# Performance work log

Measured on AMD Instinct MI355X. Metric: run time of the kernel, lower is better.

## Reference

```python
import jax, jax.numpy as jnp
import numpy as np

# Module constants (match init_kwargs)
H = 16            # num_heads
K = 64            # max_kernel_size
MAX_FREQ = 16.0
MIN_FREQ = 1.0
HALF_S = 16       # int(32**(1/1)) // 2
S = 2 * HALF_S + 1  # 33 sample offsets: -16..16
MAX_RECEPTIVE = HALF_S * MAX_FREQ  # 256.0


def setup_inputs() -> dict:
    key = jax.random.key(0)
    ks = jax.random.split(key, 6)
    B, L, C = 1, 4096, 1024
    x = jax.random.normal(ks[0], (B, L, C), dtype=jnp.float32)
    # Learned params (random small scale so offsets/kernels vary; torch inits
    # wave_proj to zeros but that degenerates the math under test).
    Ww = jax.random.normal(ks[1], (2 * H, C), dtype=jnp.float32) * 0.02
    bw = jnp.zeros((2 * H,), dtype=jnp.float32)
    Wk = jax.random.normal(ks[2], (H * K, C), dtype=jnp.float32) * 0.02
    bk = jnp.zeros((H * K,), dtype=jnp.float32)
    Wo = jax.random.normal(ks[3], (C, C), dtype=jnp.float32) * 0.02
    return {"x": x, "Ww": Ww, "bw": bw, "Wk": Wk, "bk": bk, "Wo": Wo}


def reference(x, Ww, bw, Wk, bk, Wo):
    B, L, C = x.shape
    D = C // H
    dt = x.dtype
    grid = jnp.arange(-HALF_S, HALF_S + 1, dtype=dt)  # (S,)

    # Predict per-position frequency / phase (averaged over heads)
    wp = jax.nn.silu(x @ Ww.T + bw).reshape(B, L, 2, H)
    freq = jax.nn.sigmoid(wp[:, :, 0]) * (MAX_FREQ - MIN_FREQ) + MIN_FREQ  # (B,L,H)
    phase = jnp.tanh(wp[:, :, 1]) * MAX_FREQ
    freq_avg = freq.mean(-1)    # (B,L)
    phase_avg = phase.mean(-1)  # (B,L)

    # Sample positions & gather indices
    rel_pos = grid[None, None, :] * freq_avg[..., None] + phase_avg[..., None]  # (B,L,S)
    centers = jnp.arange(L, dtype=dt)
    sample_pos = centers[None, :, None] + rel_pos                               # (B,L,S)
    valid = (sample_pos >= 0) & (sample_pos < L)
    sample_idx = jnp.clip(sample_pos.astype(jnp.int32), 0, L - 1)               # trunc toward 0, like torch .long()

    # Gather values: (B,L,S,C) -> (B,L,H,S,D)
    values = jax.vmap(lambda xf, idx: xf[idx])(x, sample_idx)
    values = values.reshape(B, L, S, H, D).transpose(0, 1, 3, 2, 4)

    # Kernel profile, linearly interpolated to sample positions
    kernel_max = jax.nn.silu(x @ Wk.T + bk).reshape(B, L, H, K)
    norm_pos = jnp.clip((rel_pos + MAX_RECEPTIVE) / (2.0 * MAX_RECEPTIVE), 0.0, 1.0)
    idx_float = norm_pos * (K - 1)                       # (B,L,S)
    idx_floor = jnp.clip(idx_float.astype(jnp.int32), 0, K - 2)
    w_ceil = (idx_float - idx_floor.astype(dt))[:, :, None, :]  # (B,L,1,S)
    w_floor = 1.0 - w_ceil
    ifl = jnp.broadcast_to(idx_floor[:, :, None, :], (B, L, H, S))
    k_floor = jnp.take_along_axis(kernel_max, ifl, axis=-1)
    k_ceil = jnp.take_along_axis(kernel_max, ifl + 1, axis=-1)
    kernel = (k_floor * w_floor + k_ceil * w_ceil) * valid[:, :, None, :].astype(dt)
    kernel = kernel / (kernel.sum(-1, keepdims=True) + 1e-8)

    out = jnp.einsum('blhsd,blhs->blhd', values, kernel).reshape(B, L, C)
    out = jax.nn.silu(out @ Wo.T)
    return out
```

## Files before the change

kernel.cpp:

```cpp
#include <hip/hip_runtime.h>
#include <math.h>

#define LDIM 4096
#define CDIM 1024
#define HDIM 16
#define KDIM 64
#define SDIM 33
#define HALF_SS 16
#define MAXF 16.0f
#define MINF 1.0f
#define MAXR 256.0f

__device__ __forceinline__ float sigmoid_np(float z) {
  float e = (float)exp(-(double)z);
  return __fdiv_rn(1.0f, __fadd_rn(1.0f, e));
}
__device__ __forceinline__ float silu_f(float z) {
  return __fmul_rn(z, sigmoid_np(z));
}

__device__ __forceinline__ float np_pairwise_sum(const float* a, int n) {
  float r[8];
#pragma unroll
  for (int j = 0; j < 8; ++j) r[j] = a[j];
  int i = 8;
  for (; i + 8 <= n; i += 8)
#pragma unroll
    for (int j = 0; j < 8; ++j) r[j] = __fadd_rn(r[j], a[i + j]);
  float res = __fadd_rn(__fadd_rn(__fadd_rn(r[0], r[1]), __fadd_rn(r[2], r[3])),
                        __fadd_rn(__fadd_rn(r[4], r[5]), __fadd_rn(r[6], r[7])));
  for (; i < n; ++i) res = __fadd_rn(res, a[i]);
  return res;
}

__global__ __launch_bounds__(256) void wave_kernel(
    const float* __restrict__ x, const float* __restrict__ Ww,
    const float* __restrict__ bw, float* __restrict__ fa, float* __restrict__ pa) {
  __shared__ float xs[CDIM];
  __shared__ float wp[2 * HDIM];
  int l = blockIdx.x;
  int tid = threadIdx.x;
  const float* xrow = x + (size_t)l * CDIM;
  for (int c = tid; c < CDIM; c += 256) xs[c] = xrow[c];
  __syncthreads();
  int j = tid >> 3, sub = tid & 7;
  const float* wrow = Ww + j * CDIM;
  double acc = 0.0;
  for (int c = sub; c < CDIM; c += 8) acc += (double)xs[c] * (double)wrow[c];
  for (int off = 4; off; off >>= 1) acc += __shfl_down(acc, off, 8);
  if (sub == 0) {
    float v32 = (float)(acc + (double)bw[j]);
    wp[j] = silu_f(v32);
  }
  __syncthreads();
  if (tid == 0) {
    float fv[HDIM], pv[HDIM];
    for (int h = 0; h < HDIM; ++h) {
      fv[h] = __fadd_rn(__fmul_rn(sigmoid_np(wp[h]), MAXF - MINF), MINF);
      float t32 = (float)tanh((double)wp[HDIM + h]);
      pv[h] = __fmul_rn(t32, MAXF);
    }
    fa[l] = __fdiv_rn(np_pairwise_sum(fv, HDIM), (float)HDIM);
    pa[l] = __fdiv_rn(np_pairwise_sum(pv, HDIM), (float)HDIM);
  }
}

__global__ __launch_bounds__(256) void gemm_bt_silu_f64(
    const float* __restrict__ A, const float* __restrict__ B,
    const float* __restrict__ bias, float* __restrict__ Cout,
    int M, int N, int Kd) {
  __shared__ double Asd[16][128];
  __shared__ double Bsd[16][64];
  int tid = threadIdx.x;
  int tx = tid & 15, ty = tid >> 4;
  int m0 = blockIdx.y * 128, n0 = blockIdx.x * 64;
  double acc[8][4] = {};
  for (int kt = 0; kt < Kd; kt += 16) {
#pragma unroll
    for (int q = 0; q < 2; ++q) {
      int e = tid + 256 * q;
      int row = e >> 2, kq = (e & 3) * 4;
      float4 va = *(const float4*)(A + (size_t)(m0 + row) * Kd + kt + kq);
      Asd[kq + 0][row] = (double)va.x; Asd[kq + 1][row] = (double)va.y;
      Asd[kq + 2][row] = (double)va.z; Asd[kq + 3][row] = (double)va.w;
    }
    {
      int row = tid >> 2, kq = (tid & 3) * 4;
      float4 vb = *(const float4*)(B + (size_t)(n0 + row) * Kd + kt + kq);
      Bsd[kq + 0][row] = (double)vb.x; Bsd[kq + 1][row] = (double)vb.y;
      Bsd[kq + 2][row] = (double)vb.z; Bsd[kq + 3][row] = (double)vb.w;
    }
    __syncthreads();
#pragma unroll
    for (int kk = 0; kk < 16; ++kk) {
      double a[8], b[4];
#pragma unroll
      for (int i = 0; i < 8; ++i) a[i] = Asd[kk][ty * 8 + i];
#pragma unroll
      for (int j2 = 0; j2 < 4; ++j2) b[j2] = Bsd[kk][tx * 4 + j2];
#pragma unroll
      for (int i = 0; i < 8; ++i)
#pragma unroll
        for (int j2 = 0; j2 < 4; ++j2) acc[i][j2] += a[i] * b[j2];
    }
    __syncthreads();
  }
#pragma unroll
  for (int i = 0; i < 8; ++i) {
    int mm = m0 + ty * 8 + i;
#pragma unroll
    for (int j2 = 0; j2 < 4; ++j2) {
      int nn = n0 + tx * 4 + j2;
      float v32 = (float)acc[i][j2];
      v32 = __fadd_rn(v32, bias[nn]);
      Cout[(size_t)mm * N + nn] = silu_f(v32);
    }
  }
}

__global__ __launch_bounds__(256) void gemm_bt_silu_f32(
    const float* __restrict__ A, const float* __restrict__ B,
    float* __restrict__ Cout, int M, int N, int Kd) {
  __shared__ float Asf[16][128];
  __shared__ float Bsf[16][128];
  int tid = threadIdx.x;
  int tx = tid & 15, ty = tid >> 4;
  int m0 = blockIdx.y * 128, n0 = blockIdx.x * 128;
  float acc[8][8] = {};
  for (int kt = 0; kt < Kd; kt += 16) {
#pragma unroll
    for (int q = 0; q < 2; ++q) {
      int e = tid + 256 * q;
      int row = e >> 2, kq = (e & 3) * 4;
      float4 va = *(const float4*)(A + (size_t)(m0 + row) * Kd + kt + kq);
      Asf[kq + 0][row] = va.x; Asf[kq + 1][row] = va.y;
      Asf[kq + 2][row] = va.z; Asf[kq + 3][row] = va.w;
      float4 vb = *(const float4*)(B + (size_t)(n0 + row) * Kd + kt + kq);
      Bsf[kq + 0][row] = vb.x; Bsf[kq + 1][row] = vb.y;
      Bsf[kq + 2][row] = vb.z; Bsf[kq + 3][row] = vb.w;
    }
    __syncthreads();
#pragma unroll
    for (int kk = 0; kk < 16; ++kk) {
      float4 a0 = *(const float4*)&Asf[kk][ty * 8];
      float4 a1 = *(const float4*)&Asf[kk][ty * 8 + 4];
      float4 b0 = *(const float4*)&Bsf[kk][tx * 8];
      float4 b1 = *(const float4*)&Bsf[kk][tx * 8 + 4];
      float a[8] = {a0.x, a0.y, a0.z, a0.w, a1.x, a1.y, a1.z, a1.w};
      float b[8] = {b0.x, b0.y, b0.z, b0.w, b1.x, b1.y, b1.z, b1.w};
#pragma unroll
      for (int i = 0; i < 8; ++i)
#pragma unroll
        for (int j2 = 0; j2 < 8; ++j2) acc[i][j2] += a[i] * b[j2];
    }
    __syncthreads();
  }
#pragma unroll
  for (int i = 0; i < 8; ++i) {
    int mm = m0 + ty * 8 + i;
#pragma unroll
    for (int j2 = 0; j2 < 8; ++j2) {
      int nn = n0 + tx * 8 + j2;
      Cout[(size_t)mm * N + nn] = silu_f(acc[i][j2]);
    }
  }
}

__global__ __launch_bounds__(256) void conv_kernel(
    const float* __restrict__ x, const float* __restrict__ km,
    const float* __restrict__ fa, const float* __restrict__ pa,
    float* __restrict__ conv) {
  int l = blockIdx.x;
  int tid = threadIdx.x;
  __shared__ int s_idx[SDIM];
  __shared__ int s_ifl[SDIM];
  __shared__ float s_wc[SDIM];
  __shared__ float s_val[SDIM];
  __shared__ float kern[HDIM][SDIM];
  __shared__ float s_den[HDIM];
  if (tid < SDIM) {
    float f = fa[l], p = pa[l];
    float rel = __fadd_rn(__fmul_rn((float)(tid - HALF_SS), f), p);
    float pos = __fadd_rn((float)l, rel);
    bool valid = (pos >= 0.f) && (pos < (float)LDIM);
    int idx = (int)pos;
    idx = min(max(idx, 0), LDIM - 1);
    s_idx[tid] = idx;
    s_val[tid] = valid ? 1.f : 0.f;
    float np_ = __fdiv_rn(__fadd_rn(rel, MAXR), 2.f * MAXR);
    np_ = fminf(fmaxf(np_, 0.f), 1.f);
    float idxf = __fmul_rn(np_, (float)(KDIM - 1));
    int ifl = (int)idxf;
    ifl = min(max(ifl, 0), KDIM - 2);
    s_ifl[tid] = ifl;
    s_wc[tid] = __fsub_rn(idxf, (float)ifl);
  }
  __syncthreads();
  for (int t = tid; t < HDIM * SDIM; t += 256) {
    int h = t / SDIM, s = t - h * SDIM;
    const float* kb = km + (size_t)l * CDIM + h * KDIM;
    float wc = s_wc[s];
    float wf = __fsub_rn(1.f, wc);
    float v = __fadd_rn(__fmul_rn(kb[s_ifl[s]], wf), __fmul_rn(kb[s_ifl[s] + 1], wc));
    kern[h][s] = __fmul_rn(v, s_val[s]);
  }
  __syncthreads();
  if (tid < HDIM) {
    float sum = np_pairwise_sum(&kern[tid][0], SDIM);
    s_den[tid] = __fadd_rn(sum, 1e-8f);
  }
  __syncthreads();
  for (int t = tid; t < HDIM * SDIM; t += 256) {
    int h = t / SDIM, s = t - h * SDIM;
    kern[h][s] = __fdiv_rn(kern[h][s], s_den[h]);
  }
  __syncthreads();
  float acc[4] = {0.f, 0.f, 0.f, 0.f};
  for (int s = 0; s < SDIM; ++s) {
    const float* xr = x + (size_t)s_idx[s] * CDIM;
#pragma unroll
    for (int q = 0; q < 4; ++q) {
      int c = tid + q * 256;
      acc[q] = __fadd_rn(acc[q], __fmul_rn(xr[c], kern[c >> 6][s]));
    }
  }
#pragma unroll
  for (int q = 0; q < 4; ++q) {
    int c = tid + q * 256;
    conv[(size_t)l * CDIM + c] = acc[q];
  }
}

extern "C" void kernel_launch(void* const* d_in, const int* in_sizes, int n_in,
                              void* d_out, int out_size, void* d_ws, size_t ws_size,
                              hipStream_t stream) {
  const float* x  = (const float*)d_in[0];
  const float* Ww = (const float*)d_in[1];
  const float* bw = (const float*)d_in[2];
  const float* Wk = (const float*)d_in[3];
  const float* bk = (const float*)d_in[4];
  const float* Wo = (const float*)d_in[5];
  float* out = (float*)d_out;

  float* fa   = (float*)d_ws;
  float* pa   = fa + LDIM;
  float* km   = pa + LDIM;
  float* conv = km + (size_t)LDIM * CDIM;

  wave_kernel<<<LDIM, 256, 0, stream>>>(x, Ww, bw, fa, pa);

  dim3 kmgrid(CDIM / 64, LDIM / 128);
  gemm_bt_silu_f64<<<kmgrid, 256, 0, stream>>>(x, Wk, bk, km, LDIM, CDIM, CDIM);

  conv_kernel<<<LDIM, 256, 0, stream>>>(x, km, fa, pa, conv);

  dim3 ogrid(CDIM / 128, LDIM / 128);
  gemm_bt_silu_f32<<<ogrid, 256, 0, stream>>>(conv, Wo, out, LDIM, CDIM, CDIM);
}
```

Baseline: 521.3 us.

## Double-buffer shared tiles and shrink GEMM tiles to 64x64 in both GEMMs

Both the f64 kernel-profile GEMM and the f32 output GEMM now use double-buffered shared-memory tiles: the next K-slice is prefetched into registers while the current one is computed, which leaves one barrier per iteration. Block tiles shrink to 64x64 with padded shared arrays and vectorized shared reads and global stores. The aim is to hide global-load latency, cut bank conflicts and put more blocks on the device. In exchange each thread does fewer FMAs per shared load, so arithmetic intensity is lower, which may hurt the f32 GEMM.

```diff
diff --git a/kernel.cpp b/kernel.cpp
--- a/kernel.cpp
+++ b/kernel.cpp
@@ -69,100 +69,143 @@
     const float* __restrict__ A, const float* __restrict__ B,
     const float* __restrict__ bias, float* __restrict__ Cout,
     int M, int N, int Kd) {
-  __shared__ double Asd[16][128];
-  __shared__ double Bsd[16][64];
+  __shared__ double Asd[2][16][66];
+  __shared__ double Bsd[2][16][66];
   int tid = threadIdx.x;
-  int tx = tid & 15, ty = tid >> 4;
-  int m0 = blockIdx.y * 128, n0 = blockIdx.x * 64;
-  double acc[8][4] = {};
-  for (int kt = 0; kt < Kd; kt += 16) {
-#pragma unroll
-    for (int q = 0; q < 2; ++q) {
-      int e = tid + 256 * q;
-      int row = e >> 2, kq = (e & 3) * 4;
-      float4 va = *(const float4*)(A + (size_t)(m0 + row) * Kd + kt + kq);
-      Asd[kq + 0][row] = (double)va.x; Asd[kq + 1][row] = (double)va.y;
-      Asd[kq + 2][row] = (double)va.z; Asd[kq + 3][row] = (double)va.w;
-    }
-    {
-      int row = tid >> 2, kq = (tid & 3) * 4;
-      float4 vb = *(const float4*)(B + (size_t)(n0 + row) * Kd + kt + kq);
-      Bsd[kq + 0][row] = (double)vb.x; Bsd[kq + 1][row] = (double)vb.y;
-      Bsd[kq + 2][row] = (double)vb.z; Bsd[kq + 3][row] = (double)vb.w;
+  int tx = tid & 31;
+  int ty = tid >> 5;
+  int m0 = blockIdx.y * 64, n0 = blockIdx.x * 64;
+
+  int rS = tid >> 2;
+  int kq = (tid & 3) * 4;
+  const float* Ag = A + (size_t)(m0 + rS) * Kd + kq;
+  const float* Bg = B + (size_t)(n0 + rS) * Kd + kq;
+
+  double acc[8][2] = {};
+
+  {
+    float4 va = *(const float4*)(Ag);
+    float4 vb = *(const float4*)(Bg);
+    Asd[0][kq + 0][rS] = (double)va.x; Asd[0][kq + 1][rS] = (double)va.y;
+    Asd[0][kq + 2][rS] = (double)va.z; Asd[0][kq + 3][rS] = (double)va.w;
+    Bsd[0][kq + 0][rS] = (double)vb.x; Bsd[0][kq + 1][rS] = (double)vb.y;
+    Bsd[0][kq + 2][rS] = (double)vb.z; Bsd[0][kq + 3][rS] = (double)vb.w;
+  }
+  __syncthreads();
+
+  const int NK = Kd >> 4;
+  for (int kt = 0; kt < NK; ++kt) {
+    int cur = kt & 1;
+    float4 va, vb;
+    bool pf = (kt + 1 < NK);
+    if (pf) {
+      va = *(const float4*)(Ag + (kt + 1) * 16);
+      vb = *(const float4*)(Bg + (kt + 1) * 16);
+    }
+#pragma unroll
+    for (int kk = 0; kk < 16; ++kk) {
+      const double2* ap = (const double2*)&Asd[cur][kk][ty * 8];
+      double2 a0 = ap[0], a1 = ap[1], a2 = ap[2], a3 = ap[3];
+      double2 bv = *(const double2*)&Bsd[cur][kk][tx * 2];
+      double a[8] = {a0.x, a0.y, a1.x, a1.y, a2.x, a2.y, a3.x, a3.y};
+#pragma unroll
+      for (int i = 0; i < 8; ++i) {
+        acc[i][0] += a[i] * bv.x;
+        acc[i][1] += a[i] * bv.y;
+      }
+    }
+    if (pf) {
+      int nxt = cur ^ 1;
+      Asd[nxt][kq + 0][rS] = (double)va.x; Asd[nxt][kq + 1][rS] = (double)va.y;
+      Asd[nxt][kq + 2][rS] = (double)va.z; Asd[nxt][kq + 3][rS] = (double)va.w;
+      Bsd[nxt][kq + 0][rS] = (double)vb.x; Bsd[nxt][kq + 1][rS] = (double)vb.y;
+      Bsd[nxt][kq + 2][rS] = (double)vb.z; Bsd[nxt][kq + 3][rS] = (double)vb.w;
     }
     __syncthreads();
-#pragma unroll
-    for (int kk = 0; kk < 16; ++kk) {
-      double a[8], b[4];
-#pragma unroll
-      for (int i = 0; i < 8; ++i) a[i] = Asd[kk][ty * 8 + i];
-#pragma unroll
-      for (int j2 = 0; j2 < 4; ++j2) b[j2] = Bsd[kk][tx * 4 + j2];
-#pragma unroll
-      for (int i = 0; i < 8; ++i)
-#pragma unroll
-        for (int j2 = 0; j2 < 4; ++j2) acc[i][j2] += a[i] * b[j2];
-    }
-    __syncthreads();
-  }
+  }
+
 #pragma unroll
   for (int i = 0; i < 8; ++i) {
     int mm = m0 + ty * 8 + i;
-#pragma unroll
-    for (int j2 = 0; j2 < 4; ++j2) {
-      int nn = n0 + tx * 4 + j2;
-      float v32 = (float)acc[i][j2];
-      v32 = __fadd_rn(v32, bias[nn]);
-      Cout[(size_t)mm * N + nn] = silu_f(v32);
-    }
+    int nn = n0 + tx * 2;
+    float v0 = (float)acc[i][0];
+    v0 = __fadd_rn(v0, bias[nn]);
+    float v1 = (float)acc[i][1];
+    v1 = __fadd_rn(v1, bias[nn + 1]);
+    float2 o;
+    o.x = silu_f(v0);
+    o.y = silu_f(v1);
+    *(float2*)&Cout[(size_t)mm * N + nn] = o;
   }
 }
 
 __global__ __launch_bounds__(256) void gemm_bt_silu_f32(
     const float* __restrict__ A, const float* __restrict__ B,
     float* __restrict__ Cout, int M, int N, int Kd) {
-  __shared__ float Asf[16][128];
-  __shared__ float Bsf[16][128];
+  __shared__ float Asf[2][16][68];
+  __shared__ float Bsf[2][16][68];
   int tid = threadIdx.x;
-  int tx = tid & 15, ty = tid >> 4;
-  int m0 = blockIdx.y * 128, n0 = blockIdx.x * 128;
-  float acc[8][8] = {};
-  for (int kt = 0; kt < Kd; kt += 16) {
-#pragma unroll
-    for (int q = 0; q < 2; ++q) {
-      int e = tid + 256 * q;
-      int row = e >> 2, kq = (e & 3) * 4;
-      float4 va = *(const float4*)(A + (size_t)(m0 + row) * Kd + kt + kq);
-      Asf[kq + 0][row] = va.x; Asf[kq + 1][row] = va.y;
-      Asf[kq + 2][row] = va.z; Asf[kq + 3][row] = va.w;
-      float4 vb = *(const float4*)(B + (size_t)(n0 + row) * Kd + kt + kq);
-      Bsf[kq + 0][row] = vb.x; Bsf[kq + 1][row] = vb.y;
-      Bsf[kq + 2][row] = vb.z; Bsf[kq + 3][row] = vb.w;
+  int tx = tid & 15;
+  int ty = tid >> 4;
+  int m0 = blockIdx.y * 64, n0 = blockIdx.x * 64;
+
+  int rS = tid >> 2;
+  int kq = (tid & 3) * 4;
+  const float* Ag = A + (size_t)(m0 + rS) * Kd + kq;
+  const float* Bg = B + (size_t)(n0 + rS) * Kd + kq;
+
+  float acc[4][4] = {};
+
+  {
+    float4 va = *(const float4*)(Ag);
+    float4 vb = *(const float4*)(Bg);
+    Asf[0][kq + 0][rS] = va.x; Asf[0][kq + 1][rS] = va.y;
+    Asf[0][kq + 2][rS] = va.z; Asf[0][kq + 3][rS] = va.w;
+    Bsf[0][kq + 0][rS] = vb.x; Bsf[0][kq + 1][rS] = vb.y;
+    Bsf[0][kq + 2][rS] = vb.z; Bsf[0][kq + 3][rS] = vb.w;
+  }
+  __syncthreads();
+
+  const int NK = Kd >> 4;
+  for (int kt = 0; kt < NK; ++kt) {
+    int cur = kt & 1;
+    float4 va, vb;
+    bool pf = (kt + 1 < NK);
+    if (pf) {
+      va = *(const float4*)(Ag + (kt + 1) * 16);
+      vb = *(const float4*)(Bg + (kt + 1) * 16);
+    }
+#pragma unroll
+    for (int kk = 0; kk < 16; ++kk) {
+      float4 af = *(const float4*)&Asf[cur][kk][ty * 4];
+      float4 bf = *(const float4*)&Bsf[cur][kk][tx * 4];
+      float a[4] = {af.x, af.y, af.z, af.w};
+      float b[4] = {bf.x, bf.y, bf.z, bf.w};
+#pragma unroll
+      for (int i = 0; i < 4; ++i)
+#pragma unroll
+        for (int j2 = 0; j2 < 4; ++j2) acc[i][j2] += a[i] * b[j2];
+    }
+    if (pf) {
+      int nxt = cur ^ 1;
+      Asf[nxt][kq + 0][rS] = va.x; Asf[nxt][kq + 1][rS] = va.y;
+      Asf[nxt][kq + 2][rS] = va.z; Asf[nxt][kq + 3][rS] = va.w;
+      Bsf[nxt][kq + 0][rS] = vb.x; Bsf[nxt][kq + 1][rS] = vb.y;
+      Bsf[nxt][kq + 2][rS] = vb.z; Bsf[nxt][kq + 3][rS] = vb.w;
     }
     __syncthreads();
-#pragma unroll
-    for (int kk = 0; kk < 16; ++kk) {
-      float4 a0 = *(const float4*)&Asf[kk][ty * 8];
-      float4 a1 = *(const float4*)&Asf[kk][ty * 8 + 4];
-      float4 b0 = *(const float4*)&Bsf[kk][tx * 8];
-      float4 b1 = *(const float4*)&Bsf[kk][tx * 8 + 4];
-      float a[8] = {a0.x, a0.y, a0.z, a0.w, a1.x, a1.y, a1.z, a1.w};
-      float b[8] = {b0.x, b0.y, b0.z, b0.w, b1.x, b1.y, b1.z, b1.w};
-#pragma unroll
-      for (int i = 0; i < 8; ++i)
-#pragma unroll
-        for (int j2 = 0; j2 < 8; ++j2) acc[i][j2] += a[i] * b[j2];
-    }
-    __syncthreads();
-  }
-#pragma unroll
-  for (int i = 0; i < 8; ++i) {
-    int mm = m0 + ty * 8 + i;
-#pragma unroll
-    for (int j2 = 0; j2 < 8; ++j2) {
-      int nn = n0 + tx * 8 + j2;
-      Cout[(size_t)mm * N + nn] = silu_f(acc[i][j2]);
-    }
+  }
+
+#pragma unroll
+  for (int i = 0; i < 4; ++i) {
+    int mm = m0 + ty * 4 + i;
+    int nn = n0 + tx * 4;
+    float4 o;
+    o.x = silu_f(acc[i][0]);
+    o.y = silu_f(acc[i][1]);
+    o.z = silu_f(acc[i][2]);
+    o.w = silu_f(acc[i][3]);
+    *(float4*)&Cout[(size_t)mm * N + nn] = o;
   }
 }
 
@@ -249,11 +292,11 @@
 
   wave_kernel<<<LDIM, 256, 0, stream>>>(x, Ww, bw, fa, pa);
 
-  dim3 kmgrid(CDIM / 64, LDIM / 128);
+  dim3 kmgrid(CDIM / 64, LDIM / 64);
   gemm_bt_silu_f64<<<kmgrid, 256, 0, stream>>>(x, Wk, bk, km, LDIM, CDIM, CDIM);
 
   conv_kernel<<<LDIM, 256, 0, stream>>>(x, km, fa, pa, conv);
 
-  dim3 ogrid(CDIM / 128, LDIM / 128);
+  dim3 ogrid(CDIM / 64, LDIM / 64);
   gemm_bt_silu_f32<<<ogrid, 256, 0, stream>>>(conv, Wo, out, LDIM, CDIM, CDIM);
 }
```

New measurement: 696.0 us. 1.33x slower.

## Use FP64 MFMA matrix cores for the kernel-profile GEMM

Applied to the files above, without the earlier changes.

Replaces the scalar double-precision FMA loop in the x·Wk GEMM with the 16x16x4 FP64 MFMA instruction. Each of the four wavefronts computes a 128x16 output strip. Tiles are staged in shared memory as fp32 with padded rows and converted to double per operand. The lane-to-element mapping of the operands and accumulators is found at runtime by running probe MFMAs on lane indices. This removes the heavy vector FP64 FMA cost, at the price of more complex indexing and the risk of a wrong layout inference.

```diff
diff --git a/kernel.cpp b/kernel.cpp
--- a/kernel.cpp
+++ b/kernel.cpp
@@ -11,6 +11,10 @@
 #define MINF 1.0f
 #define MAXR 256.0f
 
+typedef double d4 __attribute__((ext_vector_type(4)));
+
+#define MFMA_F64 __builtin_amdgcn_mfma_f64_16x16x4f64
+
 __device__ __forceinline__ float sigmoid_np(float z) {
   float e = (float)exp(-(double)z);
   return __fdiv_rn(1.0f, __fadd_rn(1.0f, e));
@@ -69,49 +73,97 @@
     const float* __restrict__ A, const float* __restrict__ B,
     const float* __restrict__ bias, float* __restrict__ Cout,
     int M, int N, int Kd) {
-  __shared__ double Asd[16][128];
-  __shared__ double Bsd[16][64];
+  __shared__ float Asf[128][36];
+  __shared__ float Bsf[64][36];
   int tid = threadIdx.x;
-  int tx = tid & 15, ty = tid >> 4;
+  int w  = tid >> 6;
+  int l  = tid & 63;
   int m0 = blockIdx.y * 128, n0 = blockIdx.x * 64;
-  double acc[8][4] = {};
-  for (int kt = 0; kt < Kd; kt += 16) {
-#pragma unroll
-    for (int q = 0; q < 2; ++q) {
-      int e = tid + 256 * q;
-      int row = e >> 2, kq = (e & 3) * 4;
-      float4 va = *(const float4*)(A + (size_t)(m0 + row) * Kd + kt + kq);
-      Asd[kq + 0][row] = (double)va.x; Asd[kq + 1][row] = (double)va.y;
-      Asd[kq + 2][row] = (double)va.z; Asd[kq + 3][row] = (double)va.w;
-    }
-    {
-      int row = tid >> 2, kq = (tid & 3) * 4;
-      float4 vb = *(const float4*)(B + (size_t)(n0 + row) * Kd + kt + kq);
-      Bsd[kq + 0][row] = (double)vb.x; Bsd[kq + 1][row] = (double)vb.y;
-      Bsd[kq + 2][row] = (double)vb.z; Bsd[kq + 3][row] = (double)vb.w;
+
+  d4 zv = (d4)(0.0);
+  double lane_d = (double)l;
+  d4 pA = MFMA_F64(lane_d, 1.0, zv, 0, 0, 0);
+  d4 pB = MFMA_F64(1.0, lane_d, zv, 0, 0, 0);
+  int sa0 = (int)pA[0], sb0 = (int)pB[0];
+  bool aH1 = ((sa0 & 3) == 0);
+  bool bH1 = ((sb0 & 3) == 0);
+  int lmA = aH1 ? (l & 15) : (l >> 2);
+  int lqA = aH1 ? (l >> 4) : (l & 3);
+  int lmB = bH1 ? (l & 15) : (l >> 2);
+  int lqB = bH1 ? (l >> 4) : (l & 3);
+  int di[4], dj[4];
+#pragma unroll
+  for (int r = 0; r < 4; ++r) {
+    int va = (int)pA[r], vb = (int)pB[r];
+    di[r] = (aH1 ? ((va - 96) >> 2) : ((va - 6) >> 4)) & 15;
+    dj[r] = (bH1 ? ((vb - 96) >> 2) : ((vb - 6) >> 4)) & 15;
+  }
+
+  d4 acc[8];
+#pragma unroll
+  for (int i = 0; i < 8; ++i) acc[i] = (d4)(0.0);
+
+  for (int kt = 0; kt < Kd; kt += 32) {
+#pragma unroll
+    for (int qi = 0; qi < 4; ++qi) {
+      int e = tid + 256 * qi;
+      int row = e >> 3, j = e & 7;
+      float4 v = *(const float4*)(A + (size_t)(m0 + row) * Kd + kt + 4 * j);
+      Asf[row][j] = v.x; Asf[row][j + 8] = v.y;
+      Asf[row][j + 16] = v.z; Asf[row][j + 24] = v.w;
+    }
+#pragma unroll
+    for (int qi = 0; qi < 2; ++qi) {
+      int e = tid + 256 * qi;
+      int row = e >> 3, j = e & 7;
+      float4 v = *(const float4*)(B + (size_t)(n0 + row) * Kd + kt + 4 * j);
+      Bsf[row][j] = v.x; Bsf[row][j + 8] = v.y;
+      Bsf[row][j + 16] = v.z; Bsf[row][j + 24] = v.w;
     }
     __syncthreads();
 #pragma unroll
-    for (int kk = 0; kk < 16; ++kk) {
-      double a[8], b[4];
-#pragma unroll
-      for (int i = 0; i < 8; ++i) a[i] = Asd[kk][ty * 8 + i];
-#pragma unroll
-      for (int j2 = 0; j2 < 4; ++j2) b[j2] = Bsd[kk][tx * 4 + j2];
-#pragma unroll
-      for (int i = 0; i < 8; ++i)
-#pragma unroll
-        for (int j2 = 0; j2 < 4; ++j2) acc[i][j2] += a[i] * b[j2];
+    for (int t = 0; t < 2; ++t) {
+      float4 bv = *(const float4*)&Bsf[16 * w + lmB][8 * lqB + 4 * t];
+      float4 av0 = *(const float4*)&Asf[lmA][8 * lqA + 4 * t];
+      float4 av1 = *(const float4*)&Asf[16 + lmA][8 * lqA + 4 * t];
+      float4 av2 = *(const float4*)&Asf[32 + lmA][8 * lqA + 4 * t];
+      float4 av3 = *(const float4*)&Asf[48 + lmA][8 * lqA + 4 * t];
+      float4 av4 = *(const float4*)&Asf[64 + lmA][8 * lqA + 4 * t];
+      float4 av5 = *(const float4*)&Asf[80 + lmA][8 * lqA + 4 * t];
+      float4 av6 = *(const float4*)&Asf[96 + lmA][8 * lqA + 4 * t];
+      float4 av7 = *(const float4*)&Asf[112 + lmA][8 * lqA + 4 * t];
+      float bs[4] = {bv.x, bv.y, bv.z, bv.w};
+      float as0[4] = {av0.x, av0.y, av0.z, av0.w};
+      float as1[4] = {av1.x, av1.y, av1.z, av1.w};
+      float as2[4] = {av2.x, av2.y, av2.z, av2.w};
+      float as3[4] = {av3.x, av3.y, av3.z, av3.w};
+      float as4[4] = {av4.x, av4.y, av4.z, av4.w};
+      float as5[4] = {av5.x, av5.y, av5.z, av5.w};
+      float as6[4] = {av6.x, av6.y, av6.z, av6.w};
+      float as7[4] = {av7.x, av7.y, av7.z, av7.w};
+#pragma unroll
+      for (int s = 0; s < 4; ++s) {
+        double bd = (double)bs[s];
+        acc[0] = MFMA_F64((double)as0[s], bd, acc[0], 0, 0, 0);
+        acc[1] = MFMA_F64((double)as1[s], bd, acc[1], 0, 0, 0);
+        acc[2] = MFMA_F64((double)as2[s], bd, acc[2], 0, 0, 0);
+        acc[3] = MFMA_F64((double)as3[s], bd, acc[3], 0, 0, 0);
+        acc[4] = MFMA_F64((double)as4[s], bd, acc[4], 0, 0, 0);
+        acc[5] = MFMA_F64((double)as5[s], bd, acc[5], 0, 0, 0);
+        acc[6] = MFMA_F64((double)as6[s], bd, acc[6], 0, 0, 0);
+        acc[7] = MFMA_F64((double)as7[s], bd, acc[7], 0, 0, 0);
+      }
     }
     __syncthreads();
   }
-#pragma unroll
-  for (int i = 0; i < 8; ++i) {
-    int mm = m0 + ty * 8 + i;
-#pragma unroll
-    for (int j2 = 0; j2 < 4; ++j2) {
-      int nn = n0 + tx * 4 + j2;
-      float v32 = (float)acc[i][j2];
+
+#pragma unroll
+  for (int mt = 0; mt < 8; ++mt) {
+#pragma unroll
+    for (int r = 0; r < 4; ++r) {
+      int mm = m0 + 16 * mt + di[r];
+      int nn = n0 + 16 * w + dj[r];
+      float v32 = (float)acc[mt][r];
       v32 = __fadd_rn(v32, bias[nn]);
       Cout[(size_t)mm * N + nn] = silu_f(v32);
     }
```

Measured after the change: 456.1 us. -12.5%, faster.
